# Performance work log

Hardware: AMD Instinct MI355X
Metric: run time of the kernel (lower is better)

Reference implementation:

```python
import jax, jax.numpy as jnp
import numpy as np

B, S, D, H = 1, 4096, 1024, 16
HD = D // H

def _w(k, std):
    return jax.random.truncated_normal(k, -3.0, 3.0, (D, D), jnp.float32) * std

def setup_inputs() -> dict:
    key = jax.random.key(0)
    kx, kq, kk, kv, ko = jax.random.split(key, 5)
    std = (2.0 / (D + D)) ** 0.5
    return {
        "x": jax.random.normal(kx, (B, S, D), jnp.float32),
        "Wq": _w(kq, std),
        "Wk": _w(kk, std),
        "Wv": _w(kv, std),
        "Wo": _w(ko, std),
    }

def reference(x, Wq, Wk, Wv, Wo):
    # projections: Linear applies W [d_out, d_in] as x @ W.T
    def split_heads(t):
        return t.reshape(B, S, H, HD).transpose(0, 2, 1, 3)  # [B,H,S,hd]
    q = split_heads(jnp.einsum('bsd,ed->bse', x, Wq))
    k = split_heads(jnp.einsum('bsd,ed->bse', x, Wk))
    v = split_heads(jnp.einsum('bsd,ed->bse', x, Wv))
    scores = jnp.einsum('bhqd,bhkd->bhqk', q, k) / (HD ** 0.5)  # [B,H,S,S]
    causal = jnp.tril(jnp.ones((S, S), bool))
    scores = jnp.where(causal, scores, -jnp.inf)
    attn = jax.nn.softmax(scores, axis=-1)
    out = jnp.einsum('bhqk,bhkd->bhqd', attn, v)  # [B,H,S,hd]
    out = out.transpose(0, 2, 1, 3).reshape(B, S, D)
    return jnp.einsum('bsd,ed->bse', out, Wo)
```

## Files before the change

kernel.cpp:

```cpp
#include <hip/hip_runtime.h>
#include <hip/hip_bf16.h>
#include <stdint.h>

constexpr int SEQ  = 4096;
constexpr int DIM  = 1024;
constexpr int NH   = 16;
constexpr int HDM  = 64;

typedef __bf16 bf16;
typedef __attribute__((ext_vector_type(4)))  float  f32x4;
typedef __attribute__((ext_vector_type(16))) float  f32x16;
typedef __attribute__((ext_vector_type(8)))  __bf16 bf16x8;
typedef __attribute__((ext_vector_type(4)))  __bf16 bf16x4;
typedef __attribute__((ext_vector_type(4)))  unsigned u32x4;

__device__ __forceinline__ void gload_lds16(const bf16* g, bf16* l) {
  __builtin_amdgcn_global_load_lds(
      (const __attribute__((address_space(1))) unsigned int*)g,
      (__attribute__((address_space(3))) unsigned int*)l, 16, 0, 0);
}

__device__ __forceinline__ unsigned pack2(float lo, float hi) {
  unsigned short a = __builtin_bit_cast(unsigned short, (bf16)lo);
  unsigned short b = __builtin_bit_cast(unsigned short, (bf16)hi);
  return ((unsigned)b << 16) | a;
}

__global__ void cvt5(const float* __restrict__ x,  const float* __restrict__ wq,
                     const float* __restrict__ wk, const float* __restrict__ wv,
                     const float* __restrict__ wo,
                     bf16* __restrict__ xb,  bf16* __restrict__ wqb,
                     bf16* __restrict__ wkb, bf16* __restrict__ wvb,
                     bf16* __restrict__ wob) {
  const float* in; bf16* out; int n;
  switch (blockIdx.y) {
    case 0:  in = x;  out = xb;  n = SEQ * DIM; break;
    case 1:  in = wq; out = wqb; n = DIM * DIM; break;
    case 2:  in = wk; out = wkb; n = DIM * DIM; break;
    case 3:  in = wv; out = wvb; n = DIM * DIM; break;
    default: in = wo; out = wob; n = DIM * DIM; break;
  }
  const int i = (blockIdx.x * blockDim.x + threadIdx.x) * 8;
  if (i >= n) return;
  f32x4 a = *(const f32x4*)(in + i);
  f32x4 b = *(const f32x4*)(in + i + 4);
  bf16x8 o;
#pragma unroll
  for (int j = 0; j < 4; ++j) { o[j] = (bf16)a[j]; o[j + 4] = (bf16)b[j]; }
  *(bf16x8*)(out + i) = o;
}

template <typename OutT, bool QKV>
__global__ __launch_bounds__(256, 2)
void gemm_xwt(const bf16* __restrict__ A,
              const bf16* __restrict__ W0, const bf16* __restrict__ W1,
              const bf16* __restrict__ W2,
              OutT* __restrict__ C0, OutT* __restrict__ C1, OutT* __restrict__ C2) {
  const bf16* W;
  OutT* C;
  float sc = 1.0f;
  if (QKV) {
    const int z = blockIdx.z;
    W = (z == 0) ? W0 : (z == 1) ? W1 : W2;
    C = (z == 0) ? C0 : (z == 1) ? C1 : C2;
    if (z == 0) sc = 0.18033688011112042f;
  } else {
    W = W0; C = C0;
  }
  __shared__ bf16 As[128 * 32];
  __shared__ bf16 Bs[128 * 32];
  const int tid = threadIdx.x;
  const int w   = tid >> 6;
  const int l   = tid & 63;
  const int l15 = l & 15, lhi = l >> 4;
  const int wr  = w >> 1, wc = w & 1;
  const int row0 = blockIdx.y * 128;
  const int col0 = blockIdx.x * 128;

  f32x4 acc[4][4] = {};

  const int srow = w * 32 + (l >> 2);
  const int scol = (l & 3) * 8;
  const bf16* gA = A + (size_t)(row0 + srow) * DIM + scol;
  const bf16* gB = W + (size_t)(col0 + srow) * DIM + scol;
  bf16* lA = As + srow * 32 + scol;
  bf16* lB = Bs + srow * 32 + scol;

  for (int k0 = 0; k0 < DIM; k0 += 32) {
    __syncthreads();
    gload_lds16(gA + k0,            lA);
    gload_lds16(gA + k0 + 16 * DIM, lA + 16 * 32);
    gload_lds16(gB + k0,            lB);
    gload_lds16(gB + k0 + 16 * DIM, lB + 16 * 32);
    __syncthreads();
    bf16x8 af[4], bf_[4];
#pragma unroll
    for (int m = 0; m < 4; ++m)
      af[m] = *(const bf16x8*)(As + (wr * 64 + m * 16 + l15) * 32 + lhi * 8);
#pragma unroll
    for (int n = 0; n < 4; ++n)
      bf_[n] = *(const bf16x8*)(Bs + (wc * 64 + n * 16 + l15) * 32 + lhi * 8);
#pragma unroll
    for (int m = 0; m < 4; ++m)
#pragma unroll
      for (int n = 0; n < 4; ++n)
        acc[m][n] = __builtin_amdgcn_mfma_f32_16x16x32_bf16(af[m], bf_[n], acc[m][n], 0, 0, 0);
  }

#pragma unroll
  for (int m = 0; m < 4; ++m)
#pragma unroll
    for (int n = 0; n < 4; ++n)
#pragma unroll
      for (int r = 0; r < 4; ++r) {
        const int row = row0 + wr * 64 + m * 16 + lhi * 4 + r;
        const int col = col0 + wc * 64 + n * 16 + l15;
        C[(size_t)row * DIM + col] = (OutT)(acc[m][n][r] * sc);
      }
}

__global__ __launch_bounds__(256, 2)
void gemm_out(const bf16* __restrict__ A, const bf16* __restrict__ W,
              float* __restrict__ C) {
  __shared__ bf16 As[64 * 32];
  __shared__ bf16 Bs[128 * 32];
  const int tid = threadIdx.x;
  const int w   = tid >> 6;
  const int l   = tid & 63;
  const int l15 = l & 15, lhi = l >> 4;
  const int wr  = w >> 1, wc = w & 1;
  const int row0 = blockIdx.y * 64;
  const int col0 = blockIdx.x * 128;

  f32x4 acc[2][4] = {};

  const int srowA = w * 16 + (l >> 2);
  const int srowB = w * 32 + (l >> 2);
  const int scol  = (l & 3) * 8;
  const bf16* gA = A + (size_t)(row0 + srowA) * DIM + scol;
  const bf16* gB = W + (size_t)(col0 + srowB) * DIM + scol;
  bf16* lA = As + srowA * 32 + scol;
  bf16* lB = Bs + srowB * 32 + scol;

  for (int k0 = 0; k0 < DIM; k0 += 32) {
    __syncthreads();
    gload_lds16(gA + k0,            lA);
    gload_lds16(gB + k0,            lB);
    gload_lds16(gB + k0 + 16 * DIM, lB + 16 * 32);
    __syncthreads();
    bf16x8 af[2], bf_[4];
#pragma unroll
    for (int m = 0; m < 2; ++m)
      af[m] = *(const bf16x8*)(As + (wr * 32 + m * 16 + l15) * 32 + lhi * 8);
#pragma unroll
    for (int n = 0; n < 4; ++n)
      bf_[n] = *(const bf16x8*)(Bs + (wc * 64 + n * 16 + l15) * 32 + lhi * 8);
#pragma unroll
    for (int m = 0; m < 2; ++m)
#pragma unroll
      for (int n = 0; n < 4; ++n)
        acc[m][n] = __builtin_amdgcn_mfma_f32_16x16x32_bf16(af[m], bf_[n], acc[m][n], 0, 0, 0);
  }

#pragma unroll
  for (int m = 0; m < 2; ++m)
#pragma unroll
    for (int n = 0; n < 4; ++n)
#pragma unroll
      for (int r = 0; r < 4; ++r) {
        const int row = row0 + wr * 32 + m * 16 + lhi * 4 + r;
        const int col = col0 + wc * 64 + n * 16 + l15;
        C[(size_t)row * DIM + col] = acc[m][n][r];
      }
}

__global__ __launch_bounds__(256)
void transpose_v(const bf16* __restrict__ Vs, bf16* __restrict__ Vt) {
  __shared__ bf16 t[64][72];
  const int st = blockIdx.x * 64;
  const int dt = blockIdx.y * 64;
  const int tid = threadIdx.x;
  const int r  = tid >> 2;
  const int c0 = (tid & 3) * 16;
  bf16x8 a = *(const bf16x8*)(Vs + (size_t)(st + r) * DIM + dt + c0);
  bf16x8 b = *(const bf16x8*)(Vs + (size_t)(st + r) * DIM + dt + c0 + 8);
#pragma unroll
  for (int j = 0; j < 8; ++j) { t[r][c0 + j] = a[j]; t[r][c0 + 8 + j] = b[j]; }
  __syncthreads();
  const int d  = tid >> 2;
  const int s0 = (tid & 3) * 16;
  bf16x8 o1, o2;
#pragma unroll
  for (int j = 0; j < 8; ++j) { o1[j] = t[s0 + j][d]; o2[j] = t[s0 + 8 + j][d]; }
  bf16* dst = Vt + (size_t)(dt + d) * SEQ + st + s0;
  *(bf16x8*)(dst)     = o1;
  *(bf16x8*)(dst + 8) = o2;
}

__global__ __launch_bounds__(256, 2)
void attn_fwd(const bf16* __restrict__ Qg, const bf16* __restrict__ Kg,
              const bf16* __restrict__ Vt,
              bf16* __restrict__ P0, bf16* __restrict__ P1,
              bf16* __restrict__ P2, bf16* __restrict__ P3,
              float* __restrict__ ms) {
  __shared__ bf16 Kl[2][8][64][8];
  __shared__ bf16 Vl[2][8][64][8];
  const int tid = threadIdx.x;
  const int wv  = tid >> 6;
  const int l   = tid & 63;
  const int l31 = l & 31;
  const int hi  = l >> 5;
  const int bid = blockIdx.x;
  const int s   = bid & 3;
  const int bh  = bid >> 2;
  const int b   = 31 - (bh >> 4);
  const int h   = bh & 15;
  const int qb0 = b * 128;
  const int hc  = h * HDM;
  const int tmaxb = 2 * b + 1;
  const int tdiag = 2 * b + (wv >> 1);
  const int qg  = qb0 + wv * 32 + l31;
  bf16* Po = (s == 0) ? P0 : (s == 1) ? P1 : (s == 2) ? P2 : P3;

  bf16x8 qf[4];
#pragma unroll
  for (int ks = 0; ks < 4; ++ks)
    qf[ks] = *(const bf16x8*)(Qg + (size_t)qg * DIM + hc + ks * 16 + hi * 8);

  f32x16 ota0 = {}, otb0 = {}, ota1 = {}, otb1 = {};
  float sacc[8] = {};

  auto stage = [&](int bb, int t) {
    const int kv0 = t * 64;
#pragma unroll
    for (int c = 0; c < 2; ++c) {
      const int p = c * 4 + wv;
      gload_lds16(Kg + (size_t)(kv0 + l) * DIM + hc + p * 8, &Kl[bb][p][0][0]);
      gload_lds16(Vt + (size_t)(hc + l) * SEQ + kv0 + p * 8, &Vl[bb][p][0][0]);
    }
  };

  if (s <= tmaxb) {
    stage(0, s);
    int bb = 0;
#pragma unroll 1
    for (int t = s; t <= tmaxb; t += 4) {
      __syncthreads();
      if (t + 4 <= tmaxb) stage(bb ^ 1, t + 4);
      if (t <= tdiag) {
        const int kv0 = t * 64;
        bf16x8 kf0[4], kf1[4];
#pragma unroll
        for (int ks = 0; ks < 4; ++ks) {
          kf0[ks] = *(const bf16x8*)&Kl[bb][ks * 2 + hi][l31][0];
          kf1[ks] = *(const bf16x8*)&Kl[bb][ks * 2 + hi][32 + l31][0];
        }
        f32x16 s0 = {}, s1 = {};
        __builtin_amdgcn_s_setprio(1);
#pragma unroll
        for (int ks = 0; ks < 4; ++ks) {
          s0 = __builtin_amdgcn_mfma_f32_32x32x16_bf16(kf0[ks], qf[ks], s0, 0, 0, 0);
          s1 = __builtin_amdgcn_mfma_f32_32x32x16_bf16(kf1[ks], qf[ks], s1, 0, 0, 0);
        }
        __builtin_amdgcn_s_setprio(0);
        bf16x8 vf0[4], vf1[4];
#pragma unroll
        for (int k2 = 0; k2 < 4; ++k2) {
          vf0[k2] = *(const bf16x8*)&Vl[bb][k2 * 2 + hi][l31][0];
          vf1[k2] = *(const bf16x8*)&Vl[bb][k2 * 2 + hi][32 + l31][0];
        }
        if (t == tdiag) {
#pragma unroll
          for (int r = 0; r < 16; ++r) {
            const int kp = (r & 3) + 8 * (r >> 2) + 4 * hi;
            if (kv0 + kp      > qg) s0[r] = -1.0e30f;
            if (kv0 + 32 + kp > qg) s1[r] = -1.0e30f;
          }
        }
#pragma unroll
        for (int r = 0; r < 16; ++r) {
          s0[r] = __builtin_exp2f(s0[r]);
          s1[r] = __builtin_exp2f(s1[r]);
        }
#pragma unroll
        for (int r = 0; r < 8; ++r)
          sacc[r] += (s0[r] + s0[r + 8]) + (s1[r] + s1[r + 8]);
        __builtin_amdgcn_s_setprio(1);
#pragma unroll
        for (int sub = 0; sub < 2; ++sub) {
#pragma unroll
          for (int hf = 0; hf < 2; ++hf) {
            const int rb = hf * 8;
            float v0, v1, v2, v3, v4, v5, v6, v7;
            if (sub == 0) {
              v0 = s0[rb+0]; v1 = s0[rb+1]; v2 = s0[rb+2]; v3 = s0[rb+3];
              v4 = s0[rb+4]; v5 = s0[rb+5]; v6 = s0[rb+6]; v7 = s0[rb+7];
            } else {
              v0 = s1[rb+0]; v1 = s1[rb+1]; v2 = s1[rb+2]; v3 = s1[rb+3];
              v4 = s1[rb+4]; v5 = s1[rb+5]; v6 = s1[rb+6]; v7 = s1[rb+7];
            }
            const unsigned w0 = pack2(v0, v1), w1 = pack2(v2, v3);
            const unsigned w2 = pack2(v4, v5), w3 = pack2(v6, v7);
            const unsigned sa = hi ? w0 : w2;
            const unsigned sb = hi ? w1 : w3;
            const unsigned ra  = (unsigned)__shfl_xor((int)sa, 32);
            const unsigned rb_ = (unsigned)__shfl_xor((int)sb, 32);
            u32x4 fu;
            fu[0] = hi ? ra  : w0;
            fu[1] = hi ? rb_ : w1;
            fu[2] = hi ? w2  : ra;
            fu[3] = hi ? w3  : rb_;
            const bf16x8 pb = __builtin_bit_cast(bf16x8, fu);
            const bf16x8 va0 = (sub == 0) ? (hf == 0 ? vf0[0] : vf0[1])
                                          : (hf == 0 ? vf0[2] : vf0[3]);
            const bf16x8 va1 = (sub == 0) ? (hf == 0 ? vf1[0] : vf1[1])
                                          : (hf == 0 ? vf1[2] : vf1[3]);
            if (sub == 0) {
              ota0 = __builtin_amdgcn_mfma_f32_32x32x16_bf16(va0, pb, ota0, 0, 0, 0);
              ota1 = __builtin_amdgcn_mfma_f32_32x32x16_bf16(va1, pb, ota1, 0, 0, 0);
            } else {
              otb0 = __builtin_amdgcn_mfma_f32_32x32x16_bf16(va0, pb, otb0, 0, 0, 0);
              otb1 = __builtin_amdgcn_mfma_f32_32x32x16_bf16(va1, pb, otb1, 0, 0, 0);
            }
          }
        }
        __builtin_amdgcn_s_setprio(0);
      }
      bb ^= 1;
    }
  }

  f32x16 ot0, ot1;
#pragma unroll
  for (int r = 0; r < 16; ++r) { ot0[r] = ota0[r] + otb0[r]; ot1[r] = ota1[r] + otb1[r]; }
  float sum_ = 0.f;
  {
    float t4[4];
#pragma unroll
    for (int r = 0; r < 4; ++r) t4[r] = sacc[r] + sacc[r + 4];
    sum_ = (t4[0] + t4[1]) + (t4[2] + t4[3]);
    sum_ += __shfl_xor(sum_, 32);
  }
#pragma unroll
  for (int g = 0; g < 4; ++g) {
    bf16x4 o0, o1;
#pragma unroll
    for (int e = 0; e < 4; ++e) {
      o0[e] = (bf16)ot0[g * 4 + e];
      o1[e] = (bf16)ot1[g * 4 + e];
    }
    *(bf16x4*)(Po + (size_t)qg * DIM + hc + g * 8 + hi * 4)      = o0;
    *(bf16x4*)(Po + (size_t)qg * DIM + hc + 32 + g * 8 + hi * 4) = o1;
  }
  if (hi == 0)
    ms[((size_t)s * SEQ + qg) * NH + h] = sum_;
}

__global__ __launch_bounds__(256)
void attn_combine(const bf16* __restrict__ P0, const bf16* __restrict__ P1,
                  const bf16* __restrict__ P2, const bf16* __restrict__ P3,
                  const float* __restrict__ ms, bf16* __restrict__ At) {
  const int idx = blockIdx.x * 256 + threadIdx.x;
  const int q  = idx >> 7;
  const int d0 = (idx & 127) * 8;
  const int h  = d0 >> 6;
  float den = 0.f;
#pragma unroll
  for (int s = 0; s < 4; ++s)
    den += ms[((size_t)s * SEQ + q) * NH + h];
  const float inv = 1.0f / den;
  const size_t off = (size_t)q * DIM + d0;
  bf16x8 p0 = *(const bf16x8*)(P0 + off);
  bf16x8 p1 = *(const bf16x8*)(P1 + off);
  bf16x8 p2 = *(const bf16x8*)(P2 + off);
  bf16x8 p3 = *(const bf16x8*)(P3 + off);
  bf16x8 o;
#pragma unroll
  for (int j = 0; j < 8; ++j) {
    const float v = (float)p0[j] + (float)p1[j] + (float)p2[j] + (float)p3[j];
    o[j] = (bf16)(v * inv);
  }
  *(bf16x8*)(At + off) = o;
}

extern "C" void kernel_launch(void* const* d_in, const int* in_sizes, int n_in,
                              void* d_out, int out_size, void* d_ws, size_t ws_size,
                              hipStream_t stream) {
  const float* x  = (const float*)d_in[0];
  const float* Wq = (const float*)d_in[1];
  const float* Wk = (const float*)d_in[2];
  const float* Wv = (const float*)d_in[3];
  const float* Wo = (const float*)d_in[4];
  float* out = (float*)d_out;

  constexpr size_t MT = (size_t)SEQ * DIM;
  bf16* xb  = (bf16*)d_ws;
  bf16* wqb = xb  + MT;
  bf16* wkb = wqb + (size_t)DIM * DIM;
  bf16* wvb = wkb + (size_t)DIM * DIM;
  bf16* wob = wvb + (size_t)DIM * DIM;
  bf16* Qs  = wob + (size_t)DIM * DIM;
  bf16* Ks  = Qs  + MT;
  bf16* Vs  = Ks  + MT;
  bf16* P1  = Vs  + MT;
  bf16* P2  = P1  + MT;
  bf16* P3  = P2  + MT;
  float* ms = (float*)(P3 + MT);
  bf16* Vt  = xb;
  bf16* P0  = Vs;
  bf16* At  = Vs;

  cvt5<<<dim3((SEQ * DIM) / (256 * 8), 5), 256, 0, stream>>>(
      x, Wq, Wk, Wv, Wo, xb, wqb, wkb, wvb, wob);

  gemm_xwt<bf16, true><<<dim3(DIM / 128, SEQ / 128, 3), 256, 0, stream>>>(
      xb, wqb, wkb, wvb, Qs, Ks, Vs);

  transpose_v<<<dim3(SEQ / 64, DIM / 64), 256, 0, stream>>>(Vs, Vt);

  attn_fwd<<<dim3(2048), 256, 0, stream>>>(Qs, Ks, Vt, P0, P1, P2, P3, ms);

  attn_combine<<<dim3((SEQ * DIM / 8) / 256), 256, 0, stream>>>(
      P0, P1, P2, P3, ms, At);

  gemm_out<<<dim3(DIM / 128, SEQ / 64), 256, 0, stream>>>(At, wob, out);
}
```

Baseline: 157.5 us.

## Fuse split-KV partial combine into output projection GEMM A-tile load

Removes the separate attn_combine pass: a tiny kernel computes per-row, per-head inverse denominators, and gemm_out sums the four bf16 partial outputs, scales them and writes the A tile to LDS itself instead of reading a combined buffer. This avoids writing and rereading the combined attention tensor. The cost is that the partials are re-read by every column block of the GEMM (8 times), and the async global-to-LDS load for A becomes a synchronous register path. Separately, attn_fwd now uses two PV accumulators instead of four, which lowers register use but lengthens the MFMA dependency chains.

```diff
diff --git a/kernel.cpp b/kernel.cpp
--- a/kernel.cpp
+++ b/kernel.cpp
@@ -116,61 +116,6 @@
         const int row = row0 + wr * 64 + m * 16 + lhi * 4 + r;
         const int col = col0 + wc * 64 + n * 16 + l15;
         C[(size_t)row * DIM + col] = (OutT)(acc[m][n][r] * sc);
-      }
-}
-
-__global__ __launch_bounds__(256, 2)
-void gemm_out(const bf16* __restrict__ A, const bf16* __restrict__ W,
-              float* __restrict__ C) {
-  __shared__ bf16 As[64 * 32];
-  __shared__ bf16 Bs[128 * 32];
-  const int tid = threadIdx.x;
-  const int w   = tid >> 6;
-  const int l   = tid & 63;
-  const int l15 = l & 15, lhi = l >> 4;
-  const int wr  = w >> 1, wc = w & 1;
-  const int row0 = blockIdx.y * 64;
-  const int col0 = blockIdx.x * 128;
-
-  f32x4 acc[2][4] = {};
-
-  const int srowA = w * 16 + (l >> 2);
-  const int srowB = w * 32 + (l >> 2);
-  const int scol  = (l & 3) * 8;
-  const bf16* gA = A + (size_t)(row0 + srowA) * DIM + scol;
-  const bf16* gB = W + (size_t)(col0 + srowB) * DIM + scol;
-  bf16* lA = As + srowA * 32 + scol;
-  bf16* lB = Bs + srowB * 32 + scol;
-
-  for (int k0 = 0; k0 < DIM; k0 += 32) {
-    __syncthreads();
-    gload_lds16(gA + k0,            lA);
-    gload_lds16(gB + k0,            lB);
-    gload_lds16(gB + k0 + 16 * DIM, lB + 16 * 32);
-    __syncthreads();
-    bf16x8 af[2], bf_[4];
-#pragma unroll
-    for (int m = 0; m < 2; ++m)
-      af[m] = *(const bf16x8*)(As + (wr * 32 + m * 16 + l15) * 32 + lhi * 8);
-#pragma unroll
-    for (int n = 0; n < 4; ++n)
-      bf_[n] = *(const bf16x8*)(Bs + (wc * 64 + n * 16 + l15) * 32 + lhi * 8);
-#pragma unroll
-    for (int m = 0; m < 2; ++m)
-#pragma unroll
-      for (int n = 0; n < 4; ++n)
-        acc[m][n] = __builtin_amdgcn_mfma_f32_16x16x32_bf16(af[m], bf_[n], acc[m][n], 0, 0, 0);
-  }
-
-#pragma unroll
-  for (int m = 0; m < 2; ++m)
-#pragma unroll
-    for (int n = 0; n < 4; ++n)
-#pragma unroll
-      for (int r = 0; r < 4; ++r) {
-        const int row = row0 + wr * 32 + m * 16 + lhi * 4 + r;
-        const int col = col0 + wc * 64 + n * 16 + l15;
-        C[(size_t)row * DIM + col] = acc[m][n][r];
       }
 }
 
@@ -227,7 +172,7 @@
   for (int ks = 0; ks < 4; ++ks)
     qf[ks] = *(const bf16x8*)(Qg + (size_t)qg * DIM + hc + ks * 16 + hi * 8);
 
-  f32x16 ota0 = {}, otb0 = {}, ota1 = {}, otb1 = {};
+  f32x16 ot0 = {}, ot1 = {};
   float sacc[8] = {};
 
   auto stage = [&](int bb, int t) {
@@ -311,17 +256,13 @@
             fu[2] = hi ? w2  : ra;
             fu[3] = hi ? w3  : rb_;
             const bf16x8 pb = __builtin_bit_cast(bf16x8, fu);
-            const bf16x8 va0 = (sub == 0) ? (hf == 0 ? vf0[0] : vf0[1])
-                                          : (hf == 0 ? vf0[2] : vf0[3]);
-            const bf16x8 va1 = (sub == 0) ? (hf == 0 ? vf1[0] : vf1[1])
-                                          : (hf == 0 ? vf1[2] : vf1[3]);
-            if (sub == 0) {
-              ota0 = __builtin_amdgcn_mfma_f32_32x32x16_bf16(va0, pb, ota0, 0, 0, 0);
-              ota1 = __builtin_amdgcn_mfma_f32_32x32x16_bf16(va1, pb, ota1, 0, 0, 0);
-            } else {
-              otb0 = __builtin_amdgcn_mfma_f32_32x32x16_bf16(va0, pb, otb0, 0, 0, 0);
-              otb1 = __builtin_amdgcn_mfma_f32_32x32x16_bf16(va1, pb, otb1, 0, 0, 0);
-            }
+            const int k2 = sub * 2 + hf;
+            ot0 = __builtin_amdgcn_mfma_f32_32x32x16_bf16(
+                k2 == 0 ? vf0[0] : k2 == 1 ? vf0[1] : k2 == 2 ? vf0[2] : vf0[3],
+                pb, ot0, 0, 0, 0);
+            ot1 = __builtin_amdgcn_mfma_f32_32x32x16_bf16(
+                k2 == 0 ? vf1[0] : k2 == 1 ? vf1[1] : k2 == 2 ? vf1[2] : vf1[3],
+                pb, ot1, 0, 0, 0);
           }
         }
         __builtin_amdgcn_s_setprio(0);
@@ -330,9 +271,6 @@
     }
   }
 
-  f32x16 ot0, ot1;
-#pragma unroll
-  for (int r = 0; r < 16; ++r) { ot0[r] = ota0[r] + otb0[r]; ot1[r] = ota1[r] + otb1[r]; }
   float sum_ = 0.f;
   {
     float t4[4];
@@ -357,30 +295,83 @@
 }
 
 __global__ __launch_bounds__(256)
-void attn_combine(const bf16* __restrict__ P0, const bf16* __restrict__ P1,
-                  const bf16* __restrict__ P2, const bf16* __restrict__ P3,
-                  const float* __restrict__ ms, bf16* __restrict__ At) {
-  const int idx = blockIdx.x * 256 + threadIdx.x;
-  const int q  = idx >> 7;
-  const int d0 = (idx & 127) * 8;
-  const int h  = d0 >> 6;
-  float den = 0.f;
-#pragma unroll
-  for (int s = 0; s < 4; ++s)
-    den += ms[((size_t)s * SEQ + q) * NH + h];
-  const float inv = 1.0f / den;
-  const size_t off = (size_t)q * DIM + d0;
-  bf16x8 p0 = *(const bf16x8*)(P0 + off);
-  bf16x8 p1 = *(const bf16x8*)(P1 + off);
-  bf16x8 p2 = *(const bf16x8*)(P2 + off);
-  bf16x8 p3 = *(const bf16x8*)(P3 + off);
-  bf16x8 o;
-#pragma unroll
-  for (int j = 0; j < 8; ++j) {
-    const float v = (float)p0[j] + (float)p1[j] + (float)p2[j] + (float)p3[j];
-    o[j] = (bf16)(v * inv);
-  }
-  *(bf16x8*)(At + off) = o;
+void attn_den(const float* __restrict__ ms, float* __restrict__ invden) {
+  const int i = blockIdx.x * 256 + threadIdx.x;
+  float d = 0.f;
+#pragma unroll
+  for (int s = 0; s < 4; ++s) d += ms[(size_t)s * SEQ * NH + i];
+  invden[i] = 1.0f / d;
+}
+
+__global__ __launch_bounds__(256, 2)
+void gemm_out(const bf16* __restrict__ P0, const bf16* __restrict__ P1,
+              const bf16* __restrict__ P2, const bf16* __restrict__ P3,
+              const float* __restrict__ invden,
+              const bf16* __restrict__ W, float* __restrict__ C) {
+  __shared__ bf16 As[64 * 32];
+  __shared__ bf16 Bs[128 * 32];
+  const int tid = threadIdx.x;
+  const int w   = tid >> 6;
+  const int l   = tid & 63;
+  const int l15 = l & 15, lhi = l >> 4;
+  const int wr  = w >> 1, wc = w & 1;
+  const int row0 = blockIdx.y * 64;
+  const int col0 = blockIdx.x * 128;
+
+  f32x4 acc[2][4] = {};
+
+  const int srowA = w * 16 + (l >> 2);
+  const int srowB = w * 32 + (l >> 2);
+  const int scol  = (l & 3) * 8;
+  const int arow  = row0 + srowA;
+  const size_t poff = (size_t)arow * DIM + scol;
+  const bf16* gB = W + (size_t)(col0 + srowB) * DIM + scol;
+  bf16* lA = As + srowA * 32 + scol;
+  bf16* lB = Bs + srowB * 32 + scol;
+
+  for (int k0 = 0; k0 < DIM; k0 += 32) {
+    __syncthreads();
+    gload_lds16(gB + k0,            lB);
+    gload_lds16(gB + k0 + 16 * DIM, lB + 16 * 32);
+    {
+      const float inv = invden[arow * NH + ((k0 + scol) >> 6)];
+      bf16x8 p0 = *(const bf16x8*)(P0 + poff + k0);
+      bf16x8 p1 = *(const bf16x8*)(P1 + poff + k0);
+      bf16x8 p2 = *(const bf16x8*)(P2 + poff + k0);
+      bf16x8 p3 = *(const bf16x8*)(P3 + poff + k0);
+      bf16x8 a;
+#pragma unroll
+      for (int j = 0; j < 8; ++j) {
+        const float v = (float)p0[j] + (float)p1[j] + (float)p2[j] + (float)p3[j];
+        a[j] = (bf16)(v * inv);
+      }
+      *(bf16x8*)lA = a;
+    }
+    __syncthreads();
+    bf16x8 af[2], bf_[4];
+#pragma unroll
+    for (int m = 0; m < 2; ++m)
+      af[m] = *(const bf16x8*)(As + (wr * 32 + m * 16 + l15) * 32 + lhi * 8);
+#pragma unroll
+    for (int n = 0; n < 4; ++n)
+      bf_[n] = *(const bf16x8*)(Bs + (wc * 64 + n * 16 + l15) * 32 + lhi * 8);
+#pragma unroll
+    for (int m = 0; m < 2; ++m)
+#pragma unroll
+      for (int n = 0; n < 4; ++n)
+        acc[m][n] = __builtin_amdgcn_mfma_f32_16x16x32_bf16(af[m], bf_[n], acc[m][n], 0, 0, 0);
+  }
+
+#pragma unroll
+  for (int m = 0; m < 2; ++m)
+#pragma unroll
+    for (int n = 0; n < 4; ++n)
+#pragma unroll
+      for (int r = 0; r < 4; ++r) {
+        const int row = row0 + wr * 32 + m * 16 + lhi * 4 + r;
+        const int col = col0 + wc * 64 + n * 16 + l15;
+        C[(size_t)row * DIM + col] = acc[m][n][r];
+      }
 }
 
 extern "C" void kernel_launch(void* const* d_in, const int* in_sizes, int n_in,
@@ -406,9 +397,9 @@
   bf16* P2  = P1  + MT;
   bf16* P3  = P2  + MT;
   float* ms = (float*)(P3 + MT);
+  float* invden = ms + (size_t)4 * SEQ * NH;
   bf16* Vt  = xb;
   bf16* P0  = Vs;
-  bf16* At  = Vs;
 
   cvt5<<<dim3((SEQ * DIM) / (256 * 8), 5), 256, 0, stream>>>(
       x, Wq, Wk, Wv, Wo, xb, wqb, wkb, wvb, wob);
@@ -420,8 +411,8 @@
 
   attn_fwd<<<dim3(2048), 256, 0, stream>>>(Qs, Ks, Vt, P0, P1, P2, P3, ms);
 
-  attn_combine<<<dim3((SEQ * DIM / 8) / 256), 256, 0, stream>>>(
-      P0, P1, P2, P3, ms, At);
-
-  gemm_out<<<dim3(DIM / 128, SEQ / 64), 256, 0, stream>>>(At, wob, out);
-}
+  attn_den<<<dim3(SEQ * NH / 256), 256, 0, stream>>>(ms, invden);
+
+  gemm_out<<<dim3(DIM / 128, SEQ / 64), 256, 0, stream>>>(
+      P0, P1, P2, P3, invden, wob, out);
+}
```

After: 169.4 us. 7.6% more time.
